# Kernel optimization log

Measured on AMD Instinct MI355X. Metric: run time of the kernel, lower is better.

Reference implementation:

```python
import jax, jax.numpy as jnp
import numpy as np
import math

B, C, H, W = 16, 512, 32, 32
NUM_HEADS = 8
EPS = 1e-5

def setup_inputs() -> dict:
    key = jax.random.key(0)
    ks = jax.random.split(key, 4)
    x = jax.random.normal(ks[0], (B, C, H, W), dtype=jnp.float32)
    emb = jax.random.normal(ks[1], (B, C), dtype=jnp.float32)
    w_qkv = jax.random.normal(ks[2], (3 * C, C), dtype=jnp.float32) * (1.0 / math.sqrt(C))
    b_qkv = jnp.zeros((3 * C,), dtype=jnp.float32)
    w_proj = jax.random.normal(ks[3], (C, C), dtype=jnp.float32) * (1.0 / math.sqrt(C))
    b_proj = jnp.zeros((C,), dtype=jnp.float32)
    return {"x": x, "emb": emb, "w_qkv": w_qkv, "b_qkv": b_qkv, "w_proj": w_proj, "b_proj": b_proj}


def reference(x, emb, w_qkv, b_qkv, w_proj, b_proj):
    b, c = x.shape[0], x.shape[1]
    spatial = x.shape[2:]
    xf = x.reshape(b, c, -1)                      # [b, c, T]
    # LayerNorm over channel dim (dim=1), no affine
    mu = jnp.mean(xf, axis=1, keepdims=True)
    var = jnp.var(xf, axis=1, keepdims=True)
    xn = (xf - mu) / jnp.sqrt(var + EPS)
    # 1x1 conv = channel GEMM: [3c,c] x [b,c,T] -> [b,3c,T]
    qkv = jnp.einsum('oc,bct->bot', w_qkv, xn) + b_qkv[None, :, None]
    T = qkv.shape[-1]
    qkv = qkv.reshape(b * NUM_HEADS, -1, T)       # [b*h, 3*hd, T]
    ch = qkv.shape[1] // 3
    q, k, v = jnp.split(qkv, 3, axis=1)
    scale = 1.0 / math.sqrt(math.sqrt(ch))
    w = jnp.einsum('bct,bcs->bts', q * scale, k * scale)  # [b*h, T, T]
    w = jax.nn.softmax(w.astype(jnp.float32), axis=-1).astype(qkv.dtype)
    h = jnp.einsum('bts,bcs->bct', w, v)          # [b*h, hd, T]
    h = h.reshape(b, -1, T)                        # [b, c, T]
    h = jnp.einsum('oc,bct->bot', w_proj, h) + b_proj[None, :, None]
    return (xf + h).reshape(b, c, *spatial)
```

## Files before the change

### kernel.cpp

```cpp
#include <hip/hip_runtime.h>


#define TSZ 1024
#define CCH 512
#define NBATCH 16

typedef __attribute__((ext_vector_type(8))) short short8;
typedef __attribute__((ext_vector_type(4))) float f32x4;
typedef __attribute__((ext_vector_type(4))) int i32x4;

__device__ inline short f2bf(float f) {
  unsigned u = __builtin_bit_cast(unsigned, f);
  u += 0x7fff + ((u >> 16) & 1);
  return (short)(u >> 16);
}

__device__ inline void gl16(const void* g, void* l) {
  __builtin_amdgcn_global_load_lds((const __attribute__((address_space(1))) void*)g,
                                   (__attribute__((address_space(3))) void*)l,
                                   16, 0, 0);
}

__global__ __launch_bounds__(256) void k_cvt(const float* __restrict__ wq,
                                             const float* __restrict__ wp,
                                             short* __restrict__ wqb,
                                             short* __restrict__ wpb) {
  int i = blockIdx.x * 256 + threadIdx.x;
  const int nq = 1536 * 512;
  if (i < nq) wqb[i] = f2bf(wq[i]);
  int j = i - nq;
  if (j >= 0 && j < 512 * 512) wpb[j] = f2bf(wp[j]);
}

__global__ __launch_bounds__(256) void k_ln(const float* __restrict__ x,
                                            short* __restrict__ xnT) {
  const int b = blockIdx.x;
  const int t0 = blockIdx.y * 64;
  const int tid = threadIdx.x;
  const int tt = tid & 63, cg = tid >> 6;

  __shared__ float red[2][4][64];
  __shared__ float mu_s[64], rs_s[64];
  __shared__ float xt[64][65];

  const float* xb = x + (long)b * CCH * TSZ;

  float s = 0.f, s2 = 0.f;
  for (int c = cg * 128; c < cg * 128 + 128; ++c) {
    float v = xb[(long)c * TSZ + t0 + tt];
    s += v; s2 += v * v;
  }
  red[0][cg][tt] = s; red[1][cg][tt] = s2;
  __syncthreads();
  if (tid < 64) {
    float ss = red[0][0][tid] + red[0][1][tid] + red[0][2][tid] + red[0][3][tid];
    float qq = red[1][0][tid] + red[1][1][tid] + red[1][2][tid] + red[1][3][tid];
    float mu = ss * (1.f / 512.f);
    float var = qq * (1.f / 512.f) - mu * mu;
    mu_s[tid] = mu;
    rs_s[tid] = rsqrtf(var + 1e-5f);
  }
  __syncthreads();

  for (int c0 = 0; c0 < CCH; c0 += 64) {
    for (int i = tid; i < 64 * 64; i += 256) {
      int ci = i >> 6, t2 = i & 63;
      xt[ci][t2] = xb[(long)(c0 + ci) * TSZ + t0 + t2];
    }
    __syncthreads();
    for (int i = tid; i < 64 * 64; i += 256) {
      int cc = i & 63, t2 = i >> 6;
      float v = (xt[cc][t2] - mu_s[t2]) * rs_s[t2];
      xnT[((long)b * TSZ + t0 + t2) * CCH + c0 + cc] = f2bf(v);
    }
    __syncthreads();
  }
}

__device__ inline int qkmap(int n) {
  if (n < 512) return (n >> 6) * 192 + (n & 63);
  int j = n - 512;
  return (j >> 6) * 192 + 64 + (j & 63);
}
__device__ inline int vmap(int m) {
  return (m >> 6) * 192 + 128 + (m & 63);
}

template <int MODE>
__global__ __launch_bounds__(256) void k_gemm(const short* __restrict__ Ab,
                                              const short* __restrict__ Bb,
                                              void* __restrict__ outb,
                                              const float* __restrict__ bias,
                                              const float* __restrict__ resid) {
  const int b = blockIdx.z;
  const int m0 = blockIdx.x * 128, n0 = blockIdx.y * 128;
  const int tid = threadIdx.x;
  const int lane = tid & 63, wv = tid >> 6;
  const int wm = wv >> 1, wn = wv & 1;
  const int l15 = lane & 15, lg = lane >> 4;

  const short* A = Ab + (MODE == 0 ? (long)b * TSZ * CCH : 0);
  const short* Bm = Bb + (MODE == 0 ? 0 : (long)b * TSZ * CCH);

  __shared__ __attribute__((aligned(16))) short sA[128 * 32];
  __shared__ __attribute__((aligned(16))) short sB[128 * 32];

  f32x4 acc[4][4];
#pragma unroll
  for (int i = 0; i < 4; ++i)
#pragma unroll
    for (int j = 0; j < 4; ++j) acc[i][j] = (f32x4){0.f, 0.f, 0.f, 0.f};

  long a_src[2], b_src[2];
#pragma unroll
  for (int q = 0; q < 2; ++q) {
    int idx = wv * 128 + q * 64 + lane;
    int row = idx >> 2, kc = (idx & 3) * 8;
    int am = m0 + row;
    int ar = (MODE == 1) ? vmap(am) : am;
    a_src[q] = (long)ar * CCH + kc;
    int bn = n0 + row;
    int br = (MODE == 0) ? qkmap(bn) : bn;
    b_src[q] = (long)br * CCH + kc;
  }

  for (int k0 = 0; k0 < CCH; k0 += 32) {
#pragma unroll
    for (int q = 0; q < 2; ++q) {
      gl16(A + a_src[q] + k0, sA + (wv * 128 + q * 64) * 8);
      gl16(Bm + b_src[q] + k0, sB + (wv * 128 + q * 64) * 8);
    }
    __syncthreads();
    short8 af[4], bfr[4];
#pragma unroll
    for (int i = 0; i < 4; ++i)
      af[i] = *(const short8*)(sA + ((wm * 64 + i * 16 + l15) * 32 + lg * 8));
#pragma unroll
    for (int j = 0; j < 4; ++j)
      bfr[j] = *(const short8*)(sB + ((wn * 64 + j * 16 + l15) * 32 + lg * 8));
#pragma unroll
    for (int i = 0; i < 4; ++i)
#pragma unroll
      for (int j = 0; j < 4; ++j)
        acc[i][j] = __builtin_amdgcn_mfma_f32_16x16x32_bf16(af[i], bfr[j], acc[i][j], 0, 0, 0);
    __syncthreads();
  }

#pragma unroll
  for (int i = 0; i < 4; ++i)
#pragma unroll
    for (int j = 0; j < 4; ++j)
#pragma unroll
      for (int r = 0; r < 4; ++r) {
        int mi = m0 + wm * 64 + i * 16 + lg * 4 + r;
        int ni = n0 + wn * 64 + j * 16 + l15;
        float val = acc[i][j][r];
        long o = (long)mi * TSZ + ni;
        if (MODE == 0) {
          val += bias[qkmap(ni)];
          if (ni < 512) val *= 0.18033688011112042f;
          ((short*)outb)[(long)b * TSZ * TSZ + o] = f2bf(val);
        } else if (MODE == 1) {
          val += bias[vmap(mi)];
          ((short*)outb)[(long)b * CCH * TSZ + o] = f2bf(val);
        } else {
          val += bias[mi] + resid[(long)b * CCH * TSZ + o];
          ((float*)outb)[(long)b * CCH * TSZ + o] = val;
        }
      }
}

__global__ __launch_bounds__(256, 4) void k_attn(const short* __restrict__ qk,
                                                 const short* __restrict__ vbuf,
                                                 short* __restrict__ hb) {
  const int wgid = blockIdx.y * gridDim.x + blockIdx.x;
  const int xcd = wgid & 7, kb = wgid >> 3;
  const int bh = xcd * 16 + (kb & 15);
  const int t0 = (kb >> 4) * 128;
  const int b = bh >> 3, h = bh & 7;
  const int tid = threadIdx.x;
  const int lane = tid & 63, w = tid >> 6;
  const int l15 = lane & 15, lg = lane >> 4;

  __shared__ __attribute__((aligned(16))) short kt[2][64 * 64];
  __shared__ __attribute__((aligned(16))) short vt[2][64 * 64];

  const short* qkb = qk + (long)b * TSZ * 1024;
  const short* vb = vbuf + (long)b * CCH * TSZ;

  short8 aq[2][2];
  {
    const short* qb = qkb + (long)(t0 + w * 32) * 1024 + h * 64;
#pragma unroll
    for (int jt = 0; jt < 2; ++jt)
#pragma unroll
      for (int kk = 0; kk < 2; ++kk)
        aq[jt][kk] = *(const short8*)(qb + (long)(jt * 16 + l15) * 1024 + kk * 32 + lg * 8);
  }

  f32x4 of[2][4];
  float lp[2] = {0.f, 0.f};
#pragma unroll
  for (int i = 0; i < 2; ++i)
#pragma unroll
    for (int nf = 0; nf < 4; ++nf) of[i][nf] = (f32x4){0.f, 0.f, 0.f, 0.f};

  const int addr0 = (((lg & 1) * 2) * 16 + l15) * 4;
  const int addr1 = (((lg & 1) * 2 + 1) * 16 + l15) * 4;
  const bool hisel = (lg >= 2);

  int srow[2], scoff[2];
#pragma unroll
  for (int q = 0; q < 2; ++q) {
    int idx = w * 128 + q * 64 + lane;
    int row = idx >> 3;
    int byo = ((idx & 7) * 16) ^ ((row & 7) << 4);
    srow[q] = row;
    scoff[q] = byo >> 1;
  }

#define STAGE(buf, s0s)                                                        \
  {                                                                            \
    _Pragma("unroll") for (int q = 0; q < 2; ++q) {                            \
      gl16(qkb + (long)((s0s) + srow[q]) * 1024 + 512 + h * 64 + scoff[q],     \
           kt[buf] + (w * 128 + q * 64) * 8);                                  \
      gl16(vb + ((long)(h * 64 + srow[q])) * TSZ + (s0s) + scoff[q],           \
           vt[buf] + (w * 128 + q * 64) * 8);                                  \
    }                                                                          \
  }

  STAGE(0, 0);
  __syncthreads();

  for (int s0 = 0; s0 < TSZ; s0 += 64) {
    const int cur = (s0 >> 6) & 1;
    if (s0 + 64 < TSZ) STAGE(cur ^ 1, s0 + 64);

    f32x4 sf[2][4];
#pragma unroll
    for (int jt = 0; jt < 2; ++jt)
#pragma unroll
      for (int ms = 0; ms < 4; ++ms) sf[jt][ms] = (f32x4){0.f, 0.f, 0.f, 0.f};
#pragma unroll
    for (int kk = 0; kk < 2; ++kk)
#pragma unroll
      for (int ms = 0; ms < 4; ++ms) {
        int srw = ms * 16 + l15;
        int byo = ((srw * 64 + kk * 32 + lg * 8) * 2) ^ ((srw & 7) << 4);
        short8 ka = *(const short8*)((const char*)kt[cur] + byo);
#pragma unroll
        for (int jt = 0; jt < 2; ++jt)
          sf[jt][ms] = __builtin_amdgcn_mfma_f32_16x16x32_bf16(ka, aq[jt][kk], sf[jt][ms], 0, 0, 0);
      }

    short8 apf[2][2];
#pragma unroll
    for (int jt = 0; jt < 2; ++jt) {
      float p[4][4];
#pragma unroll
      for (int ms = 0; ms < 4; ++ms)
#pragma unroll
        for (int r = 0; r < 4; ++r)
          p[ms][r] = exp2f(sf[jt][ms][r]);
#pragma unroll
      for (int ms = 0; ms < 4; ++ms)
        lp[jt] += (p[ms][0] + p[ms][1]) + (p[ms][2] + p[ms][3]);
      unsigned pk[4][2];
#pragma unroll
      for (int ms = 0; ms < 4; ++ms)
#pragma unroll
        for (int u = 0; u < 2; ++u)
          asm("v_cvt_pk_bf16_f32 %0, %1, %2" : "=v"(pk[ms][u])
              : "v"(p[ms][2 * u]), "v"(p[ms][2 * u + 1]));
#pragma unroll
      for (int kk = 0; kk < 2; ++kk) {
        i32x4 a32;
#pragma unroll
        for (int j2 = 0; j2 < 4; ++j2) {
          int addr = (j2 & 2) ? addr1 : addr0;
          int lo = __builtin_amdgcn_ds_bpermute(addr, (int)pk[2 * kk][j2 & 1]);
          int hi = __builtin_amdgcn_ds_bpermute(addr, (int)pk[2 * kk + 1][j2 & 1]);
          a32[j2] = hisel ? hi : lo;
        }
        apf[jt][kk] = __builtin_bit_cast(short8, a32);
      }
    }

#pragma unroll
    for (int kk = 0; kk < 2; ++kk)
#pragma unroll
      for (int nf = 0; nf < 4; ++nf) {
        int cc = nf * 16 + l15;
        int byo = ((cc * 64 + kk * 32 + lg * 8) * 2) ^ ((cc & 7) << 4);
        short8 bv = *(const short8*)((const char*)vt[cur] + byo);
#pragma unroll
        for (int i = 0; i < 2; ++i)
          of[i][nf] = __builtin_amdgcn_mfma_f32_16x16x32_bf16(apf[i][kk], bv, of[i][nf], 0, 0, 0);
      }
    __syncthreads();
  }

  float linv[2][4];
#pragma unroll
  for (int i = 0; i < 2; ++i) {
    float ls = lp[i];
    ls += __shfl_xor(ls, 16);
    ls += __shfl_xor(ls, 32);
#pragma unroll
    for (int r = 0; r < 4; ++r)
      linv[i][r] = 1.0f / __shfl(ls, lg * 4 + r);
  }

#pragma unroll
  for (int i = 0; i < 2; ++i)
#pragma unroll
    for (int nf = 0; nf < 4; ++nf)
#pragma unroll
      for (int r = 0; r < 4; ++r) {
        int t = t0 + w * 32 + i * 16 + lg * 4 + r;
        int c = h * 64 + nf * 16 + l15;
        hb[((long)b * TSZ + t) * CCH + c] = f2bf(of[i][nf][r] * linv[i][r]);
      }
}

extern "C" void kernel_launch(void* const* d_in, const int* in_sizes, int n_in,
                              void* d_out, int out_size, void* d_ws, size_t ws_size,
                              hipStream_t stream) {
  const float* x = (const float*)d_in[0];
  const float* wq = (const float*)d_in[2];
  const float* bq = (const float*)d_in[3];
  const float* wp = (const float*)d_in[4];
  const float* bp = (const float*)d_in[5];

  char* ws = (char*)d_ws;
  short* wqb = (short*)ws;  ws += (long)1536 * 512 * 2;
  short* wpb = (short*)ws;  ws += (long)512 * 512 * 2;
  short* xnT = (short*)ws;  ws += (long)NBATCH * TSZ * CCH * 2;
  short* qkb = (short*)ws;  ws += (long)NBATCH * TSZ * 1024 * 2;
  short* vb  = (short*)ws;  ws += (long)NBATCH * CCH * TSZ * 2;
  short* hbuf = xnT;

  k_cvt<<<4096, 256, 0, stream>>>(wq, wp, wqb, wpb);
  k_ln<<<dim3(NBATCH, 16), 256, 0, stream>>>(x, xnT);
  k_gemm<0><<<dim3(8, 8, NBATCH), 256, 0, stream>>>(xnT, wqb, qkb, bq, nullptr);
  k_gemm<1><<<dim3(4, 8, NBATCH), 256, 0, stream>>>(wqb, xnT, vb, bq, nullptr);
  k_attn<<<dim3(8, 128), 256, 0, stream>>>(qkb, vb, hbuf);
  k_gemm<2><<<dim3(4, 8, NBATCH), 256, 0, stream>>>(wpb, hbuf, d_out, bp, x);
}
```

Before: 252.9 us.

## Permute V tile in LDS to drop bpermute shuffles of softmax probabilities

Result: faster. 245.1 us (-3.1%).

```diff
diff --git a/kernel.cpp b/kernel.cpp
--- a/kernel.cpp
+++ b/kernel.cpp
@@ -8,6 +8,8 @@
 typedef __attribute__((ext_vector_type(8))) short short8;
 typedef __attribute__((ext_vector_type(4))) float f32x4;
 typedef __attribute__((ext_vector_type(4))) int i32x4;
+typedef __attribute__((ext_vector_type(4))) unsigned u32x4;
+typedef __attribute__((ext_vector_type(2))) unsigned u32x2;
 
 __device__ inline short f2bf(float f) {
   unsigned u = __builtin_bit_cast(unsigned, f);
@@ -205,10 +207,6 @@
 #pragma unroll
     for (int nf = 0; nf < 4; ++nf) of[i][nf] = (f32x4){0.f, 0.f, 0.f, 0.f};
 
-  const int addr0 = (((lg & 1) * 2) * 16 + l15) * 4;
-  const int addr1 = (((lg & 1) * 2 + 1) * 16 + l15) * 4;
-  const bool hisel = (lg >= 2);
-
   int srow[2], scoff[2];
 #pragma unroll
   for (int q = 0; q < 2; ++q) {
@@ -219,22 +217,43 @@
     scoff[q] = byo >> 1;
   }
 
-#define STAGE(buf, s0s)                                                        \
+  long vsrc[2];
+  int vdstA[2], vdstB[2];
+#pragma unroll
+  for (int q = 0; q < 2; ++q) {
+    int idx = q * 256 + tid;
+    int c = idx >> 3, s8 = (idx & 7) * 8;
+    vsrc[q] = (long)(h * 64 + c) * TSZ + s8;
+    int kk2 = s8 >> 5, h4 = (s8 >> 4) & 1, lgf0 = (s8 & 15) >> 2;
+    int spA = kk2 * 32 + lgf0 * 8 + h4 * 4;
+    vdstA[q] = ((c * 64 + spA) * 2) ^ ((c & 7) << 4);
+    vdstB[q] = ((c * 64 + spA + 8) * 2) ^ ((c & 7) << 4);
+  }
+
+#define STAGE_K(buf, s0s)                                                      \
   {                                                                            \
-    _Pragma("unroll") for (int q = 0; q < 2; ++q) {                            \
+    _Pragma("unroll") for (int q = 0; q < 2; ++q)                              \
       gl16(qkb + (long)((s0s) + srow[q]) * 1024 + 512 + h * 64 + scoff[q],     \
            kt[buf] + (w * 128 + q * 64) * 8);                                  \
-      gl16(vb + ((long)(h * 64 + srow[q])) * TSZ + (s0s) + scoff[q],           \
-           vt[buf] + (w * 128 + q * 64) * 8);                                  \
-    }                                                                          \
-  }
-
-  STAGE(0, 0);
+  }
+
+  u32x4 vreg0 = *(const u32x4*)(vb + vsrc[0]);
+  u32x4 vreg1 = *(const u32x4*)(vb + vsrc[1]);
+  STAGE_K(0, 0);
+  *(u32x2*)((char*)vt[0] + vdstA[0]) = (u32x2){vreg0.x, vreg0.y};
+  *(u32x2*)((char*)vt[0] + vdstB[0]) = (u32x2){vreg0.z, vreg0.w};
+  *(u32x2*)((char*)vt[0] + vdstA[1]) = (u32x2){vreg1.x, vreg1.y};
+  *(u32x2*)((char*)vt[0] + vdstB[1]) = (u32x2){vreg1.z, vreg1.w};
   __syncthreads();
 
   for (int s0 = 0; s0 < TSZ; s0 += 64) {
     const int cur = (s0 >> 6) & 1;
-    if (s0 + 64 < TSZ) STAGE(cur ^ 1, s0 + 64);
+    const bool np = (s0 + 64 < TSZ);
+    if (np) {
+      vreg0 = *(const u32x4*)(vb + vsrc[0] + s0 + 64);
+      vreg1 = *(const u32x4*)(vb + vsrc[1] + s0 + 64);
+      STAGE_K(cur ^ 1, s0 + 64);
+    }
 
     f32x4 sf[2][4];
 #pragma unroll
@@ -274,14 +293,8 @@
               : "v"(p[ms][2 * u]), "v"(p[ms][2 * u + 1]));
 #pragma unroll
       for (int kk = 0; kk < 2; ++kk) {
-        i32x4 a32;
-#pragma unroll
-        for (int j2 = 0; j2 < 4; ++j2) {
-          int addr = (j2 & 2) ? addr1 : addr0;
-          int lo = __builtin_amdgcn_ds_bpermute(addr, (int)pk[2 * kk][j2 & 1]);
-          int hi = __builtin_amdgcn_ds_bpermute(addr, (int)pk[2 * kk + 1][j2 & 1]);
-          a32[j2] = hisel ? hi : lo;
-        }
+        i32x4 a32 = (i32x4){(int)pk[2 * kk][0], (int)pk[2 * kk][1],
+                            (int)pk[2 * kk + 1][0], (int)pk[2 * kk + 1][1]};
         apf[jt][kk] = __builtin_bit_cast(short8, a32);
       }
     }
@@ -297,6 +310,13 @@
         for (int i = 0; i < 2; ++i)
           of[i][nf] = __builtin_amdgcn_mfma_f32_16x16x32_bf16(apf[i][kk], bv, of[i][nf], 0, 0, 0);
       }
+
+    if (np) {
+      *(u32x2*)((char*)vt[cur ^ 1] + vdstA[0]) = (u32x2){vreg0.x, vreg0.y};
+      *(u32x2*)((char*)vt[cur ^ 1] + vdstB[0]) = (u32x2){vreg0.z, vreg0.w};
+      *(u32x2*)((char*)vt[cur ^ 1] + vdstA[1]) = (u32x2){vreg1.x, vreg1.y};
+      *(u32x2*)((char*)vt[cur ^ 1] + vdstB[1]) = (u32x2){vreg1.z, vreg1.w};
+    }
     __syncthreads();
   }
 
```
